# Kernel tuning notes

Hardware: AMD Instinct MI355X
Metric: run time of the kernel (lower is better)

## Reference

```python
import jax, jax.numpy as jnp
import numpy as np

N = 50000
IN_CH = 256
HID = 16
HEADS = 4
OUT_CH = 40
E = 800000
NEG_SLOPE = 0.2


def gat_layer(x, src, dst, W, a_src, a_dst, b, heads, out_ch, concat):
    n = x.shape[0]
    h = (x @ W).reshape(n, heads, out_ch)               # [N, H, C]
    al_src = jnp.einsum('nhc,hc->nh', h, a_src)          # [N, H]
    al_dst = jnp.einsum('nhc,hc->nh', h, a_dst)
    e = jax.nn.leaky_relu(al_src[src] + al_dst[dst], NEG_SLOPE)  # [E, H]
    m = jax.ops.segment_max(e, dst, num_segments=n)      # per-dst max for stability
    e = jnp.exp(e - m[dst])
    denom = jax.ops.segment_sum(e, dst, num_segments=n)
    alpha = e / (denom[dst] + 1e-16)                     # segment softmax [E, H]
    msg = h[src] * alpha[:, :, None]                     # [E, H, C]
    out = jax.ops.segment_sum(msg, dst, num_segments=n)  # [N, H, C]
    out = out.reshape(n, heads * out_ch) if concat else out.mean(axis=1)
    return out + b


def setup_inputs() -> dict:
    key = jax.random.key(0)
    ks = jax.random.split(key, 10)
    glorot = lambda k, shape: jax.random.normal(k, shape, jnp.float32) * np.sqrt(2.0 / (shape[0] + shape[-1]))
    return {
        'x': jax.random.normal(ks[0], (N, IN_CH), jnp.float32),
        'edge_index': jax.random.randint(ks[1], (2, E), 0, N, jnp.int64),
        'W1': glorot(ks[2], (IN_CH, HEADS * HID)),
        'a_src1': glorot(ks[3], (HEADS, HID)),
        'a_dst1': glorot(ks[4], (HEADS, HID)),
        'b1': jnp.zeros((HEADS * HID,), jnp.float32),
        'W2': glorot(ks[5], (HEADS * HID, OUT_CH)),
        'a_src2': glorot(ks[6], (1, OUT_CH)),
        'a_dst2': glorot(ks[7], (1, OUT_CH)),
        'b2': jnp.zeros((OUT_CH,), jnp.float32),
    }


def reference(x, edge_index, W1, a_src1, a_dst1, b1, W2, a_src2, a_dst2, b2):
    n = x.shape[0]
    loops = jnp.arange(n, dtype=edge_index.dtype)
    src = jnp.concatenate([edge_index[0], loops])  # PyG GATConv adds self-loops
    dst = jnp.concatenate([edge_index[1], loops])
    h = gat_layer(x, src, dst, W1, a_src1, a_dst1, b1, HEADS, HID, concat=True)
    h = jax.nn.elu(h)
    out = gat_layer(h, src, dst, W2, a_src2, a_dst2, b2, 1, OUT_CH, concat=False)
    return jax.nn.log_softmax(out, axis=-1)
```

## Files before the change

kernel.cpp:

```cpp
#include <hip/hip_runtime.h>
#include <math.h>

static constexpr int IN_CH  = 256;
static constexpr int HD1    = 64;
static constexpr int HEADS  = 4;
static constexpr int OUT_CH = 40;
static constexpr float NEG  = 0.2f;
static constexpr int BSH    = 7;
static constexpr int BRNG   = 128;

typedef __attribute__((ext_vector_type(8))) short bf16x8;
typedef __attribute__((ext_vector_type(4))) short s16x4;
typedef __attribute__((ext_vector_type(4))) float f32x4;

static __device__ __forceinline__ short f2bf(float f) {
    union { float f; unsigned u; } v; v.f = f;
    unsigned r = v.u + 0x7FFFu + ((v.u >> 16) & 1u);
    return (short)(r >> 16);
}
static __device__ __forceinline__ float bf2f(unsigned short u) {
    union { unsigned u; float f; } v; v.u = ((unsigned)u) << 16;
    return v.f;
}

__global__ __launch_bounds__(256) void k_zero(int* __restrict__ bmeta, int B) {
    int t = blockIdx.x * 256 + threadIdx.x;
    if (t < B + 2) bmeta[t] = 0;
}

__global__ __launch_bounds__(256) void k_bhist(const int* __restrict__ dst, int* __restrict__ bcnt,
                                               int E, int B, int perBlk) {
    __shared__ int lcnt[4096];
    for (int i = threadIdx.x; i < B; i += 256) lcnt[i] = 0;
    __syncthreads();
    const int s0 = blockIdx.x * perBlk;
    const int s1 = min(s0 + perBlk, E);
    for (int i = s0 + threadIdx.x; i < s1; i += 256)
        atomicAdd(&lcnt[dst[i] >> BSH], 1);
    __syncthreads();
    for (int i = threadIdx.x; i < B; i += 256)
        if (lcnt[i]) atomicAdd(&bcnt[i], lcnt[i]);
}

__global__ __launch_bounds__(256) void k_balloc(const int* __restrict__ bcnt, int* __restrict__ ebstart,
        int* __restrict__ ebcur, int* __restrict__ sstart, int* __restrict__ totals, int B, int n) {
    int t = blockIdx.x * 256 + threadIdx.x;
    if (t < B) {
        int ec = bcnt[t];
        int nodes = min(n - (t << BSH), BRNG);
        ebstart[t] = atomicAdd(&totals[0], ec);
        ebcur[t]   = ebstart[t];
        sstart[t]  = atomicAdd(&totals[1], ec + nodes);
    }
}

__global__ __launch_bounds__(256) void k_bpart(const int* __restrict__ ei, int* __restrict__ ebcur,
        uint2* __restrict__ ebuf, int E, int B, int perBlk) {
    __shared__ int lcnt[4096];
    __shared__ int lofs[4096];
    for (int i = threadIdx.x; i < B; i += 256) lcnt[i] = 0;
    __syncthreads();
    const int s0 = blockIdx.x * perBlk;
    const int s1 = min(s0 + perBlk, E);
    for (int i = s0 + threadIdx.x; i < s1; i += 256)
        atomicAdd(&lcnt[ei[E + i] >> BSH], 1);
    __syncthreads();
    for (int i = threadIdx.x; i < B; i += 256) {
        const int c = lcnt[i];
        lofs[i] = c ? atomicAdd(&ebcur[i], c) : 0;
        lcnt[i] = 0;
    }
    __syncthreads();
    for (int i = s0 + threadIdx.x; i < s1; i += 256) {
        const int d = ei[E + i], s = ei[i];
        const int b = d >> BSH;
        const int r = atomicAdd(&lcnt[b], 1);
        ebuf[lofs[b] + r] = make_uint2((unsigned)s, (unsigned)d);
    }
}

__global__ __launch_bounds__(256) void k_bcsr(const uint2* __restrict__ ebuf,
        const int* __restrict__ ebstart, const int* __restrict__ bcnt, const int* __restrict__ sstart,
        int* __restrict__ rowstart, int* __restrict__ counts, int* __restrict__ ssrc, int n) {
    __shared__ int ncnt[BRNG], rloc[BRNG], cur[BRNG];
    const int b = blockIdx.x;
    const int t = threadIdx.x;
    const int n0 = b << BSH;
    const int nodes = min(n - n0, BRNG);
    const int ec = bcnt[b];
    const int e0 = ebstart[b];
    const int s0 = sstart[b];

    if (t < BRNG) ncnt[t] = (t < nodes) ? 1 : 0;
    __syncthreads();
    for (int i = t; i < ec; i += 256)
        atomicAdd(&ncnt[ebuf[e0 + i].y & (BRNG - 1)], 1);
    __syncthreads();

    if (t < BRNG) rloc[t] = ncnt[t];
    __syncthreads();
    #pragma unroll
    for (int off = 1; off < BRNG; off <<= 1) {
        int u = 0;
        if (t < BRNG && t >= off) u = rloc[t - off];
        __syncthreads();
        if (t < BRNG) rloc[t] += u;
        __syncthreads();
    }

    if (t < nodes) {
        const int ex = rloc[t] - ncnt[t];
        rowstart[n0 + t] = s0 + ex;
        counts[n0 + t]   = ncnt[t];
        ssrc[s0 + ex]    = n0 + t;
        cur[t] = ex + 1;
    }
    __syncthreads();
    for (int i = t; i < ec; i += 256) {
        const uint2 e = ebuf[e0 + i];
        const int lo = (int)e.y & (BRNG - 1);
        const int p = atomicAdd(&cur[lo], 1);
        ssrc[s0 + p] = (int)e.x;
    }
}

__global__ __launch_bounds__(256) void k_xform1(const float* __restrict__ x,
        const float* __restrict__ W1, const float* __restrict__ a_src, const float* __restrict__ a_dst,
        unsigned short* __restrict__ h1b, float* __restrict__ alsrc, float* __restrict__ aldst, int n)
{
    __shared__ short W1T[64][264];
    const int t = threadIdx.x;
    const int l = t & 63;
    const int w = t >> 6;

    {
        const int c = l;
        #pragma unroll
        for (int i = 0; i < 16; ++i) {
            const int kb = i * 16 + w * 4;
            s16x4 pk;
            pk[0] = f2bf(W1[(kb + 0) * 64 + c]);
            pk[1] = f2bf(W1[(kb + 1) * 64 + c]);
            pk[2] = f2bf(W1[(kb + 2) * 64 + c]);
            pk[3] = f2bf(W1[(kb + 3) * 64 + c]);
            *(s16x4*)&W1T[c][kb] = pk;
        }
    }
    __syncthreads();

    const int r0 = blockIdx.x * 64 + w * 16;
    const int lr = l & 15;
    const int lk = l >> 4;

    f32x4 acc[4];
    #pragma unroll
    for (int ct = 0; ct < 4; ++ct) acc[ct] = (f32x4){0.f, 0.f, 0.f, 0.f};

    int rowA = r0 + lr; if (rowA > n - 1) rowA = n - 1;
    const float* xrow = x + (size_t)rowA * IN_CH + lk * 8;

    float4 a0 = *(const float4*)(xrow);
    float4 a1 = *(const float4*)(xrow + 4);

    for (int ks = 0; ks < 8; ++ks) {
        bf16x8 bfrag[4];
        #pragma unroll
        for (int ct = 0; ct < 4; ++ct)
            bfrag[ct] = *(const bf16x8*)&W1T[ct * 16 + lr][ks * 32 + lk * 8];

        const float4 c0 = a0, c1 = a1;
        if (ks < 7) {
            a0 = *(const float4*)(xrow + (ks + 1) * 32);
            a1 = *(const float4*)(xrow + (ks + 1) * 32 + 4);
        }
        bf16x8 afrag;
        afrag[0] = f2bf(c0.x); afrag[1] = f2bf(c0.y);
        afrag[2] = f2bf(c0.z); afrag[3] = f2bf(c0.w);
        afrag[4] = f2bf(c1.x); afrag[5] = f2bf(c1.y);
        afrag[6] = f2bf(c1.z); afrag[7] = f2bf(c1.w);

        #pragma unroll
        for (int ct = 0; ct < 4; ++ct)
            acc[ct] = __builtin_amdgcn_mfma_f32_16x16x32_bf16(afrag, bfrag[ct], acc[ct], 0, 0, 0);
    }

    #pragma unroll
    for (int ct = 0; ct < 4; ++ct) {
        #pragma unroll
        for (int reg = 0; reg < 4; ++reg) {
            const int row = r0 + lk * 4 + reg;
            if (row < n) h1b[(size_t)row * HD1 + ct * 16 + lr] = (unsigned short)f2bf(acc[ct][reg]);
        }
    }

    float asv[4], adv[4];
    #pragma unroll
    for (int ct = 0; ct < 4; ++ct) { asv[ct] = a_src[ct * 16 + lr]; adv[ct] = a_dst[ct * 16 + lr]; }

    #pragma unroll
    for (int reg = 0; reg < 4; ++reg) {
        const int row = r0 + lk * 4 + reg;
        #pragma unroll
        for (int ct = 0; ct < 4; ++ct) {
            float s1 = acc[ct][reg] * asv[ct];
            float s2 = acc[ct][reg] * adv[ct];
            s1 += __shfl_xor(s1, 1); s1 += __shfl_xor(s1, 2);
            s1 += __shfl_xor(s1, 4); s1 += __shfl_xor(s1, 8);
            s2 += __shfl_xor(s2, 1); s2 += __shfl_xor(s2, 2);
            s2 += __shfl_xor(s2, 4); s2 += __shfl_xor(s2, 8);
            if (lr == 0 && row < n) {
                alsrc[row * HEADS + ct] = s1;
                aldst[row * HEADS + ct] = s2;
            }
        }
    }
}

__global__ __launch_bounds__(256) void k_aggr1(const unsigned short* __restrict__ h1b,
        const float* __restrict__ alsrc, const float* __restrict__ aldst, const float* __restrict__ b1,
        const int* __restrict__ rowstart, const int* __restrict__ counts, const int* __restrict__ ssrc,
        float* __restrict__ hact, int n)
{
    const int wid  = (blockIdx.x * blockDim.x + threadIdx.x) >> 6;
    const int lane = threadIdx.x & 63;
    const int sub  = lane & 15;
    const int head = sub >> 2;

    int nid = wid * 4 + (lane >> 4);
    const bool valid = nid < n;
    if (!valid) nid = n - 1;

    const int rs  = rowstart[nid];
    const int cnt = valid ? counts[nid] : 0;

    int maxcnt = cnt;
    maxcnt = max(maxcnt, __shfl_xor(maxcnt, 16));
    maxcnt = max(maxcnt, __shfl_xor(maxcnt, 32));

    float m = -1e30f;
    {
        const float adA = aldst[nid * HEADS + (sub & 3)];
        const int npairs = cnt * 4, maxpairs = maxcnt * 4;
        for (int idx = sub; idx < maxpairs; idx += 16) {
            if (idx < npairs) {
                int s = ssrc[rs + (idx >> 2)];
                uint2 pf = *(const uint2*)(h1b + (size_t)s * HD1 + ((idx & 3) << 4));
                asm volatile("" :: "v"(pf.x), "v"(pf.y));
                float l = alsrc[s * HEADS + (sub & 3)] + adA;
                l = l > 0.f ? l : NEG * l;
                m = fmaxf(m, l);
            }
        }
        #pragma unroll
        for (int off = 1; off < 16; off <<= 1) m = fmaxf(m, __shfl_xor(m, off));
    }

    const float adB = aldst[nid * HEADS + head];
    float d = 0.f;
    float4 acc = make_float4(0.f, 0.f, 0.f, 0.f);
    for (int i0 = 0; i0 < maxcnt; i0 += 4) {
        int  sv[4]; bool on[4];
        #pragma unroll
        for (int u = 0; u < 4; ++u) {
            const int i = i0 + u;
            on[u] = i < cnt;
            sv[u] = on[u] ? ssrc[rs + i] : 0;
        }
        ushort4 hv[4]; float lv[4];
        #pragma unroll
        for (int u = 0; u < 4; ++u) {
            hv[u] = *(const ushort4*)(h1b + (size_t)sv[u] * HD1 + sub * 4);
            lv[u] = alsrc[sv[u] * HEADS + head];
        }
        #pragma unroll
        for (int u = 0; u < 4; ++u) {
            float l = lv[u] + adB;
            l = l > 0.f ? l : NEG * l;
            const float p = on[u] ? __expf(l - m) : 0.f;
            d += p;
            acc.x = fmaf(p, bf2f(hv[u].x), acc.x);
            acc.y = fmaf(p, bf2f(hv[u].y), acc.y);
            acc.z = fmaf(p, bf2f(hv[u].z), acc.z);
            acc.w = fmaf(p, bf2f(hv[u].w), acc.w);
        }
    }

    const float inv = 1.f / (d + 1e-16f);
    const float4 bv = *(const float4*)(b1 + sub * 4);
    float4 v;
    v.x = acc.x * inv + bv.x;  v.y = acc.y * inv + bv.y;
    v.z = acc.z * inv + bv.z;  v.w = acc.w * inv + bv.w;
    v.x = v.x > 0.f ? v.x : __expf(v.x) - 1.f;
    v.y = v.y > 0.f ? v.y : __expf(v.y) - 1.f;
    v.z = v.z > 0.f ? v.z : __expf(v.z) - 1.f;
    v.w = v.w > 0.f ? v.w : __expf(v.w) - 1.f;
    if (valid) *(float4*)(hact + (size_t)nid * HD1 + sub * 4) = v;
}

__global__ __launch_bounds__(64) void k_xform2(const float* __restrict__ hin,
        const float* __restrict__ W2, const float* __restrict__ a_src, const float* __restrict__ a_dst,
        unsigned short* __restrict__ h2b, float* __restrict__ alsrc, float* __restrict__ aldst, int n)
{
    __shared__ float Ws[HD1 * OUT_CH];
    const int t = threadIdx.x;
    #pragma unroll
    for (int i = 0; i < 10; ++i) ((float4*)Ws)[i * 64 + t] = ((const float4*)W2)[i * 64 + t];
    __syncthreads();

    const int r = blockIdx.x * 64 + t;
    if (r >= n) return;

    float acc[OUT_CH];
    #pragma unroll
    for (int j = 0; j < OUT_CH; ++j) acc[j] = 0.f;

    const float4* hr = (const float4*)(hin + (size_t)r * HD1);
    for (int kq = 0; kq < 16; ++kq) {
        const float4 xv = hr[kq];
        #pragma unroll
        for (int kk = 0; kk < 4; ++kk) {
            const float xs = (kk == 0) ? xv.x : (kk == 1) ? xv.y : (kk == 2) ? xv.z : xv.w;
            const float* wrow = Ws + (kq * 4 + kk) * OUT_CH;
            #pragma unroll
            for (int jq = 0; jq < 10; ++jq) {
                const float4 w = *(const float4*)(wrow + jq * 4);
                acc[jq * 4 + 0] = fmaf(xs, w.x, acc[jq * 4 + 0]);
                acc[jq * 4 + 1] = fmaf(xs, w.y, acc[jq * 4 + 1]);
                acc[jq * 4 + 2] = fmaf(xs, w.z, acc[jq * 4 + 2]);
                acc[jq * 4 + 3] = fmaf(xs, w.w, acc[jq * 4 + 3]);
            }
        }
    }

    float s1 = 0.f, s2 = 0.f;
    #pragma unroll
    for (int jq = 0; jq < 10; ++jq) {
        const float4 av = ((const float4*)a_src)[jq];
        const float4 dv = ((const float4*)a_dst)[jq];
        s1 += acc[jq*4+0] * av.x + acc[jq*4+1] * av.y + acc[jq*4+2] * av.z + acc[jq*4+3] * av.w;
        s2 += acc[jq*4+0] * dv.x + acc[jq*4+1] * dv.y + acc[jq*4+2] * dv.z + acc[jq*4+3] * dv.w;
        ushort4 pk;
        pk.x = (unsigned short)f2bf(acc[jq*4+0]);
        pk.y = (unsigned short)f2bf(acc[jq*4+1]);
        pk.z = (unsigned short)f2bf(acc[jq*4+2]);
        pk.w = (unsigned short)f2bf(acc[jq*4+3]);
        *(ushort4*)(h2b + (size_t)r * OUT_CH + jq * 4) = pk;
    }
    alsrc[r] = s1;
    aldst[r] = s2;
}

__global__ __launch_bounds__(256) void k_aggr2(const unsigned short* __restrict__ h2b,
        const float* __restrict__ alsrc, const float* __restrict__ aldst, const float* __restrict__ b2,
        const int* __restrict__ rowstart, const int* __restrict__ counts, const int* __restrict__ ssrc,
        float* __restrict__ out, int n)
{
    const int wid  = (blockIdx.x * blockDim.x + threadIdx.x) >> 6;
    const int lane = threadIdx.x & 63;
    const int sub  = lane & 15;
    const bool act = sub < 10;
    const int subc = act ? sub : 0;

    int nid = wid * 4 + (lane >> 4);
    const bool valid = nid < n;
    if (!valid) nid = n - 1;

    const int rs  = rowstart[nid];
    const int cnt = valid ? counts[nid] : 0;

    int maxcnt = cnt;
    maxcnt = max(maxcnt, __shfl_xor(maxcnt, 16));
    maxcnt = max(maxcnt, __shfl_xor(maxcnt, 32));

    const float ad = aldst[nid];

    float m = -1e30f;
    for (int e = sub; e < maxcnt; e += 16) {
        if (e < cnt) {
            int s = ssrc[rs + e];
            uint2 pf = *(const uint2*)(h2b + (size_t)s * OUT_CH + (e & 1) * 32);
            asm volatile("" :: "v"(pf.x), "v"(pf.y));
            float l = alsrc[s] + ad;
            l = l > 0.f ? l : NEG * l;
            m = fmaxf(m, l);
        }
    }
    #pragma unroll
    for (int off = 1; off < 16; off <<= 1) m = fmaxf(m, __shfl_xor(m, off));

    float d = 0.f;
    float4 acc = make_float4(0.f, 0.f, 0.f, 0.f);
    for (int i0 = 0; i0 < maxcnt; i0 += 4) {
        int  sv[4]; bool on[4];
        #pragma unroll
        for (int u = 0; u < 4; ++u) {
            const int i = i0 + u;
            on[u] = i < cnt;
            sv[u] = on[u] ? ssrc[rs + i] : 0;
        }
        ushort4 hv[4]; float lv[4];
        #pragma unroll
        for (int u = 0; u < 4; ++u) {
            hv[u] = *(const ushort4*)(h2b + (size_t)sv[u] * OUT_CH + subc * 4);
            lv[u] = alsrc[sv[u]];
        }
        #pragma unroll
        for (int u = 0; u < 4; ++u) {
            float l = lv[u] + ad;
            l = l > 0.f ? l : NEG * l;
            const float p = on[u] ? __expf(l - m) : 0.f;
            d += p;
            acc.x = fmaf(p, bf2f(hv[u].x), acc.x);
            acc.y = fmaf(p, bf2f(hv[u].y), acc.y);
            acc.z = fmaf(p, bf2f(hv[u].z), acc.z);
            acc.w = fmaf(p, bf2f(hv[u].w), acc.w);
        }
    }

    const float inv = 1.f / (d + 1e-16f);
    const float4 bv = *(const float4*)(b2 + subc * 4);
    float4 v;
    v.x = acc.x * inv + bv.x;  v.y = acc.y * inv + bv.y;
    v.z = acc.z * inv + bv.z;  v.w = acc.w * inv + bv.w;

    float mv = act ? fmaxf(fmaxf(v.x, v.y), fmaxf(v.z, v.w)) : -1e30f;
    #pragma unroll
    for (int off = 1; off < 16; off <<= 1) mv = fmaxf(mv, __shfl_xor(mv, off));
    float ex = act ? (__expf(v.x - mv) + __expf(v.y - mv) + __expf(v.z - mv) + __expf(v.w - mv)) : 0.f;
    #pragma unroll
    for (int off = 1; off < 16; off <<= 1) ex += __shfl_xor(ex, off);
    const float lse = mv + __logf(ex);

    if (valid && act) {
        *(float4*)(out + (size_t)nid * OUT_CH + sub * 4) =
            make_float4(v.x - lse, v.y - lse, v.z - lse, v.w - lse);
    }
}

extern "C" void kernel_launch(void* const* d_in, const int* in_sizes, int n_in,
                              void* d_out, int out_size, void* d_ws, size_t ws_size,
                              hipStream_t stream) {
    const float* x      = (const float*)d_in[0];
    const int*   ei     = (const int*)d_in[1];
    const float* W1     = (const float*)d_in[2];
    const float* a_src1 = (const float*)d_in[3];
    const float* a_dst1 = (const float*)d_in[4];
    const float* b1     = (const float*)d_in[5];
    const float* W2     = (const float*)d_in[6];
    const float* a_src2 = (const float*)d_in[7];
    const float* a_dst2 = (const float*)d_in[8];
    const float* b2     = (const float*)d_in[9];
    float* out = (float*)d_out;

    const int N = in_sizes[0] / IN_CH;
    const int E = in_sizes[1] / 2;
    const int B = (N + BRNG - 1) >> BSH;

    char* p = (char*)d_ws;
    auto alloc = [&](size_t bytes) -> void* {
        void* r = (void*)p;
        p += (bytes + 255) & ~(size_t)255;
        return r;
    };
    int*   counts   = (int*)alloc((size_t)N * 4);
    int*   rowstart = (int*)alloc((size_t)N * 4);
    int*   ssrc     = (int*)alloc((size_t)(E + N) * 4);
    int*   bmeta    = (int*)alloc((size_t)(B + 2) * 4);
    int*   ebstart  = (int*)alloc((size_t)B * 4);
    int*   ebcur    = (int*)alloc((size_t)B * 4);
    int*   sstart   = (int*)alloc((size_t)B * 4);
    unsigned short* h1b = (unsigned short*)alloc((size_t)N * HD1 * 2);
    unsigned short* h2b = (unsigned short*)alloc((size_t)N * OUT_CH * 2);
    float* alsrc1   = (float*)alloc((size_t)N * HEADS * 4);
    float* aldst1   = (float*)alloc((size_t)N * HEADS * 4);
    float* hact     = (float*)alloc((size_t)N * HD1 * 4);
    uint2* ebuf     = (uint2*)hact;
    int* bcnt   = bmeta;
    int* totals = bmeta + B;
    float* alsrc2 = alsrc1; float* aldst2 = aldst1;

    const int perBlk = 8192;
    const int nblkE  = (E + perBlk - 1) / perBlk;
    const int nblk64 = (N + 63) / 64;
    const int nblkAg = (N + 15) / 16;

    k_zero  <<<(B + 2 + 255) / 256, 256, 0, stream>>>(bmeta, B);
    k_bhist <<<nblkE, 256, 0, stream>>>(ei + E, bcnt, E, B, perBlk);
    k_balloc<<<(B + 255) / 256, 256, 0, stream>>>(bcnt, ebstart, ebcur, sstart, totals, B, N);
    k_bpart <<<nblkE, 256, 0, stream>>>(ei, ebcur, ebuf, E, B, perBlk);
    k_bcsr  <<<B, 256, 0, stream>>>(ebuf, ebstart, bcnt, sstart, rowstart, counts, ssrc, N);

    k_xform1 <<<nblk64, 256, 0, stream>>>(x, W1, a_src1, a_dst1, h1b, alsrc1, aldst1, N);
    k_aggr1  <<<nblkAg, 256, 0, stream>>>(h1b, alsrc1, aldst1, b1, rowstart, counts, ssrc, hact, N);
    k_xform2 <<<nblk64, 64, 0, stream>>>(hact, W2, a_src2, a_dst2, h2b, alsrc2, aldst2, N);
    k_aggr2  <<<nblkAg, 256, 0, stream>>>(h2b, alsrc2, aldst2, b2, rowstart, counts, ssrc, out, N);
}
```

Baseline: 158.1 us.

## Split layer-1 aggregation into two half-head passes and drop gather prefetches

The layer-1 aggregation kernel is split into two launches. Each launch handles two heads (32 channels), so the per-pass gather working set of h1b is halved and is more likely to stay cache-resident. The first pass computes the per-node softmax max and stores it in a new buffer, which the second pass reads back. Separately, the dummy prefetch loads of feature rows during the max pass are removed from both aggregation kernels. The cost is an extra launch, plus the edge indices and attention logits being read twice; losing the prefetch may also reduce cache warming for the later gather.

```diff
diff --git a/kernel.cpp b/kernel.cpp
--- a/kernel.cpp
+++ b/kernel.cpp
@@ -216,15 +216,15 @@
     }
 }
 
-__global__ __launch_bounds__(256) void k_aggr1(const unsigned short* __restrict__ h1b,
+__global__ __launch_bounds__(256) void k_aggr1a(const unsigned short* __restrict__ h1b,
         const float* __restrict__ alsrc, const float* __restrict__ aldst, const float* __restrict__ b1,
         const int* __restrict__ rowstart, const int* __restrict__ counts, const int* __restrict__ ssrc,
-        float* __restrict__ hact, int n)
+        float* __restrict__ mbuf, float* __restrict__ hact, int n)
 {
     const int wid  = (blockIdx.x * blockDim.x + threadIdx.x) >> 6;
     const int lane = threadIdx.x & 63;
     const int sub  = lane & 15;
-    const int head = sub >> 2;
+    const int head = sub >> 3;
 
     int nid = wid * 4 + (lane >> 4);
     const bool valid = nid < n;
@@ -244,8 +244,6 @@
         for (int idx = sub; idx < maxpairs; idx += 16) {
             if (idx < npairs) {
                 int s = ssrc[rs + (idx >> 2)];
-                uint2 pf = *(const uint2*)(h1b + (size_t)s * HD1 + ((idx & 3) << 4));
-                asm volatile("" :: "v"(pf.x), "v"(pf.y));
                 float l = alsrc[s * HEADS + (sub & 3)] + adA;
                 l = l > 0.f ? l : NEG * l;
                 m = fmaxf(m, l);
@@ -254,10 +252,11 @@
         #pragma unroll
         for (int off = 1; off < 16; off <<= 1) m = fmaxf(m, __shfl_xor(m, off));
     }
+    if (valid && sub == 0) mbuf[nid] = m;
 
     const float adB = aldst[nid * HEADS + head];
     float d = 0.f;
-    float4 acc = make_float4(0.f, 0.f, 0.f, 0.f);
+    float2 acc = make_float2(0.f, 0.f);
     for (int i0 = 0; i0 < maxcnt; i0 += 4) {
         int  sv[4]; bool on[4];
         #pragma unroll
@@ -266,10 +265,10 @@
             on[u] = i < cnt;
             sv[u] = on[u] ? ssrc[rs + i] : 0;
         }
-        ushort4 hv[4]; float lv[4];
-        #pragma unroll
-        for (int u = 0; u < 4; ++u) {
-            hv[u] = *(const ushort4*)(h1b + (size_t)sv[u] * HD1 + sub * 4);
+        ushort2 hv[4]; float lv[4];
+        #pragma unroll
+        for (int u = 0; u < 4; ++u) {
+            hv[u] = *(const ushort2*)(h1b + (size_t)sv[u] * HD1 + sub * 2);
             lv[u] = alsrc[sv[u] * HEADS + head];
         }
         #pragma unroll
@@ -280,21 +279,75 @@
             d += p;
             acc.x = fmaf(p, bf2f(hv[u].x), acc.x);
             acc.y = fmaf(p, bf2f(hv[u].y), acc.y);
-            acc.z = fmaf(p, bf2f(hv[u].z), acc.z);
-            acc.w = fmaf(p, bf2f(hv[u].w), acc.w);
         }
     }
 
     const float inv = 1.f / (d + 1e-16f);
-    const float4 bv = *(const float4*)(b1 + sub * 4);
-    float4 v;
+    const float2 bv = *(const float2*)(b1 + sub * 2);
+    float2 v;
     v.x = acc.x * inv + bv.x;  v.y = acc.y * inv + bv.y;
-    v.z = acc.z * inv + bv.z;  v.w = acc.w * inv + bv.w;
     v.x = v.x > 0.f ? v.x : __expf(v.x) - 1.f;
     v.y = v.y > 0.f ? v.y : __expf(v.y) - 1.f;
-    v.z = v.z > 0.f ? v.z : __expf(v.z) - 1.f;
-    v.w = v.w > 0.f ? v.w : __expf(v.w) - 1.f;
-    if (valid) *(float4*)(hact + (size_t)nid * HD1 + sub * 4) = v;
+    if (valid) *(float2*)(hact + (size_t)nid * HD1 + sub * 2) = v;
+}
+
+__global__ __launch_bounds__(256) void k_aggr1b(const unsigned short* __restrict__ h1b,
+        const float* __restrict__ alsrc, const float* __restrict__ aldst, const float* __restrict__ b1,
+        const int* __restrict__ rowstart, const int* __restrict__ counts, const int* __restrict__ ssrc,
+        const float* __restrict__ mbuf, float* __restrict__ hact, int n)
+{
+    const int wid  = (blockIdx.x * blockDim.x + threadIdx.x) >> 6;
+    const int lane = threadIdx.x & 63;
+    const int sub  = lane & 15;
+    const int head = 2 + (sub >> 3);
+
+    int nid = wid * 4 + (lane >> 4);
+    const bool valid = nid < n;
+    if (!valid) nid = n - 1;
+
+    const int rs  = rowstart[nid];
+    const int cnt = valid ? counts[nid] : 0;
+
+    int maxcnt = cnt;
+    maxcnt = max(maxcnt, __shfl_xor(maxcnt, 16));
+    maxcnt = max(maxcnt, __shfl_xor(maxcnt, 32));
+
+    const float m = mbuf[nid];
+    const float adB = aldst[nid * HEADS + head];
+    float d = 0.f;
+    float2 acc = make_float2(0.f, 0.f);
+    for (int i0 = 0; i0 < maxcnt; i0 += 4) {
+        int  sv[4]; bool on[4];
+        #pragma unroll
+        for (int u = 0; u < 4; ++u) {
+            const int i = i0 + u;
+            on[u] = i < cnt;
+            sv[u] = on[u] ? ssrc[rs + i] : 0;
+        }
+        ushort2 hv[4]; float lv[4];
+        #pragma unroll
+        for (int u = 0; u < 4; ++u) {
+            hv[u] = *(const ushort2*)(h1b + (size_t)sv[u] * HD1 + 32 + sub * 2);
+            lv[u] = alsrc[sv[u] * HEADS + head];
+        }
+        #pragma unroll
+        for (int u = 0; u < 4; ++u) {
+            float l = lv[u] + adB;
+            l = l > 0.f ? l : NEG * l;
+            const float p = on[u] ? __expf(l - m) : 0.f;
+            d += p;
+            acc.x = fmaf(p, bf2f(hv[u].x), acc.x);
+            acc.y = fmaf(p, bf2f(hv[u].y), acc.y);
+        }
+    }
+
+    const float inv = 1.f / (d + 1e-16f);
+    const float2 bv = *(const float2*)(b1 + 32 + sub * 2);
+    float2 v;
+    v.x = acc.x * inv + bv.x;  v.y = acc.y * inv + bv.y;
+    v.x = v.x > 0.f ? v.x : __expf(v.x) - 1.f;
+    v.y = v.y > 0.f ? v.y : __expf(v.y) - 1.f;
+    if (valid) *(float2*)(hact + (size_t)nid * HD1 + 32 + sub * 2) = v;
 }
 
 __global__ __launch_bounds__(64) void k_xform2(const float* __restrict__ hin,
@@ -378,8 +431,6 @@
     for (int e = sub; e < maxcnt; e += 16) {
         if (e < cnt) {
             int s = ssrc[rs + e];
-            uint2 pf = *(const uint2*)(h2b + (size_t)s * OUT_CH + (e & 1) * 32);
-            asm volatile("" :: "v"(pf.x), "v"(pf.y));
             float l = alsrc[s] + ad;
             l = l > 0.f ? l : NEG * l;
             m = fmaxf(m, l);
@@ -469,6 +520,7 @@
     int*   ebstart  = (int*)alloc((size_t)B * 4);
     int*   ebcur    = (int*)alloc((size_t)B * 4);
     int*   sstart   = (int*)alloc((size_t)B * 4);
+    float* mbuf     = (float*)alloc((size_t)N * 4);
     unsigned short* h1b = (unsigned short*)alloc((size_t)N * HD1 * 2);
     unsigned short* h2b = (unsigned short*)alloc((size_t)N * OUT_CH * 2);
     float* alsrc1   = (float*)alloc((size_t)N * HEADS * 4);
@@ -491,7 +543,8 @@
     k_bcsr  <<<B, 256, 0, stream>>>(ebuf, ebstart, bcnt, sstart, rowstart, counts, ssrc, N);
 
     k_xform1 <<<nblk64, 256, 0, stream>>>(x, W1, a_src1, a_dst1, h1b, alsrc1, aldst1, N);
-    k_aggr1  <<<nblkAg, 256, 0, stream>>>(h1b, alsrc1, aldst1, b1, rowstart, counts, ssrc, hact, N);
+    k_aggr1a <<<nblkAg, 256, 0, stream>>>(h1b, alsrc1, aldst1, b1, rowstart, counts, ssrc, mbuf, hact, N);
+    k_aggr1b <<<nblkAg, 256, 0, stream>>>(h1b, alsrc1, aldst1, b1, rowstart, counts, ssrc, mbuf, hact, N);
     k_xform2 <<<nblk64, 64, 0, stream>>>(hact, W2, a_src2, a_dst2, h2b, alsrc2, aldst2, N);
     k_aggr2  <<<nblkAg, 256, 0, stream>>>(h2b, alsrc2, aldst2, b2, rowstart, counts, ssrc, out, N);
 }
```

Result: slower. 162.7 us (+2.9%).
